# Optimization experiments

Hardware: AMD Instinct MI355X
Metric: run time of the kernel (lower is better)

The kernel has to match this reference:

```python
import jax, jax.numpy as jnp
import numpy as np

N = 8192
D = 512


def setup_inputs() -> dict:
    key = jax.random.key(0)
    ks = jax.random.split(key, 6)
    s = 1.0 / np.sqrt(D)
    return {
        "x": jax.random.normal(ks[0], (N, D), jnp.float32),
        "spatial_encoding": jax.random.normal(ks[1], (N, N), jnp.float32),
        "edge_encoding": jax.random.normal(ks[2], (N, N), jnp.float32),
        "Wq": jax.random.normal(ks[3], (D, D), jnp.float32) * s,
        "bq": jnp.zeros((D,), jnp.float32),
        "Wk": jax.random.normal(ks[4], (D, D), jnp.float32) * s,
        "bk": jnp.zeros((D,), jnp.float32),
        "Wv": jax.random.normal(ks[5], (D, D), jnp.float32) * s,
        "bv": jnp.zeros((D,), jnp.float32),
    }


def reference(x, spatial_encoding, edge_encoding, Wq, bq, Wk, bk, Wv, bv):
    # Linear layers (torch nn.Linear: y = x @ W.T + b)
    q = x @ Wq.T + bq  # [N, D]
    k = x @ Wk.T + bk  # [N, D]
    v = x @ Wv.T + bv  # [N, D]
    scale = 1.0 / jnp.sqrt(jnp.asarray(q.shape[-1], q.dtype))
    a = (q @ k.T) * scale + spatial_encoding + edge_encoding  # [N, N]
    attn = jax.nn.softmax(a, axis=-1)
    return attn @ v  # [N, D]
```

## Files before the change

### kernel.cpp

```cpp
#include <hip/hip_runtime.h>


constexpr int NT = 8192;
constexpr int DM = 512;
constexpr float SM_SHIFT = 12.0f;
constexpr float QSCALE = 0.04419417382415922f;

typedef _Float16 f16;
typedef _Float16 half8  __attribute__((ext_vector_type(8)));
typedef _Float16 half4v __attribute__((ext_vector_type(4)));
typedef float    float4v __attribute__((ext_vector_type(4)));

__device__ __forceinline__ void gload_lds16(const void* gsrc, void* ldst) {
  __builtin_amdgcn_global_load_lds(
      (const __attribute__((address_space(1))) void*)gsrc,
      (__attribute__((address_space(3))) void*)ldst, 16, 0, 0);
}

template<int ROWS>
__device__ __forceinline__ void stage32(const f16* __restrict__ g, int ldg,
                                        f16* l, int tid) {
  constexpr int ITERS = (ROWS * 4) / 256;
  #pragma unroll
  for (int c = 0; c < ITERS; ++c) {
    int lin = c * 256 + tid;
    gload_lds16(g + (size_t)(lin >> 2) * ldg + (lin & 3) * 8, l + lin * 8);
  }
}

__global__ __launch_bounds__(256) void k0_convert(
    const float* __restrict__ x, const float* __restrict__ wq,
    const float* __restrict__ wk, const float* __restrict__ wv,
    f16* __restrict__ xh, f16* __restrict__ wh) {
  int i = (blockIdx.x * 256 + threadIdx.x) * 4;
  const float* src; f16* dst; int off;
  if (i < NT * DM) { src = x; dst = xh; off = i; }
  else {
    int t = i - NT * DM;
    int w = t >> 18;
    off = t & ((1 << 18) - 1);
    src = (w == 0) ? wq : (w == 1) ? wk : wv;
    dst = wh + ((size_t)w << 18);
  }
  float4v v = *(const float4v*)(src + off);
  half4v h = { (f16)v.x, (f16)v.y, (f16)v.z, (f16)v.w };
  *(half4v*)(dst + off) = h;
}

__global__ __launch_bounds__(256) void k1_qkv(
    const f16* __restrict__ xh, const f16* __restrict__ wh,
    const float* __restrict__ bq, const float* __restrict__ bk,
    const float* __restrict__ bv,
    f16* __restrict__ qh, f16* __restrict__ kh, f16* __restrict__ vh) {
  __shared__ f16 As[128 * 32], Bs[128 * 32];
  int tid = threadIdx.x;
  int z = blockIdx.z;
  const f16* B0 = wh + (size_t)z * DM * DM;
  const float* bias = (z == 0) ? bq : (z == 1) ? bk : bv;
  f16* outp = (z == 0) ? qh : (z == 1) ? kh : vh;
  float scale = (z == 0) ? QSCALE : 1.0f;
  int i0 = blockIdx.y * 128, j0 = blockIdx.x * 128;
  int lane = tid & 63, warp = tid >> 6;
  int l15 = lane & 15, quad = lane >> 4;
  int wm = (warp >> 1) * 64, wn = (warp & 1) * 64;

  float4v acc[4][4] = {};
  const f16* Ag = xh + (size_t)i0 * DM;
  const f16* Bg = B0 + (size_t)j0 * DM;
  for (int kk = 0; kk < DM; kk += 32) {
    stage32<128>(Ag + kk, DM, As, tid);
    stage32<128>(Bg + kk, DM, Bs, tid);
    __syncthreads();
    half8 a[4], b[4];
    #pragma unroll
    for (int f = 0; f < 4; ++f)
      a[f] = *(const half8*)&As[(wm + f * 16 + l15) * 32 + quad * 8];
    #pragma unroll
    for (int f = 0; f < 4; ++f)
      b[f] = *(const half8*)&Bs[(wn + f * 16 + l15) * 32 + quad * 8];
    #pragma unroll
    for (int fm = 0; fm < 4; ++fm)
      #pragma unroll
      for (int fn = 0; fn < 4; ++fn)
        acc[fm][fn] = __builtin_amdgcn_mfma_f32_16x16x32_f16(
            a[fm], b[fn], acc[fm][fn], 0, 0, 0);
    __syncthreads();
  }
  #pragma unroll
  for (int fm = 0; fm < 4; ++fm)
    #pragma unroll
    for (int r = 0; r < 4; ++r) {
      int grow = i0 + wm + fm * 16 + quad * 4 + r;
      #pragma unroll
      for (int fn = 0; fn < 4; ++fn) {
        int gcol = j0 + wn + fn * 16 + l15;
        float v = (acc[fm][fn][r] + bias[gcol]) * scale;
        outp[(size_t)grow * DM + gcol] = (f16)v;
      }
    }
}

__global__ __launch_bounds__(256) void k15_transpose(
    const f16* __restrict__ v, f16* __restrict__ vT) {
  __shared__ f16 t[64][65];
  int bj = blockIdx.x * 64;
  int bi = blockIdx.y * 64;
  int tx = threadIdx.x & 63, ty = threadIdx.x >> 6;
  #pragma unroll
  for (int i = 0; i < 16; ++i)
    t[ty + i * 4][tx] = v[(size_t)(bi + ty + i * 4) * DM + bj + tx];
  __syncthreads();
  #pragma unroll
  for (int i = 0; i < 16; ++i)
    vT[(size_t)(bj + ty + i * 4) * NT + bi + tx] = t[tx][ty + i * 4];
}

constexpr int SLD = 132;

template<bool P16>
__global__ __launch_bounds__(256) void k2_scores(
    const f16* __restrict__ qh, const f16* __restrict__ kh,
    const float* __restrict__ spatial, const float* edge,
    f16* pOut16, float* pOut32, float* __restrict__ rowsum) {
  __shared__ __align__(16) char smem[32 * SLD * 4];
  f16* As = (f16*)smem;
  f16* Bs = (f16*)(smem + 8192);
  float* slab = (float*)smem;

  int tid = threadIdx.x;
  int i0 = blockIdx.y * 128, j0 = blockIdx.x * 128;
  int lane = tid & 63, warp = tid >> 6;
  int l15 = lane & 15, quad = lane >> 4;
  int wm = (warp >> 1) * 64, wn = (warp & 1) * 64;

  float4v acc[4][4] = {};
  const f16* Ag = qh + (size_t)i0 * DM;
  const f16* Bg = kh + (size_t)j0 * DM;
  for (int kk = 0; kk < DM; kk += 32) {
    stage32<128>(Ag + kk, DM, As, tid);
    stage32<128>(Bg + kk, DM, Bs, tid);
    __syncthreads();
    half8 a[4], b[4];
    #pragma unroll
    for (int f = 0; f < 4; ++f)
      a[f] = *(const half8*)&As[(wm + f * 16 + l15) * 32 + quad * 8];
    #pragma unroll
    for (int f = 0; f < 4; ++f)
      b[f] = *(const half8*)&Bs[(wn + f * 16 + l15) * 32 + quad * 8];
    #pragma unroll
    for (int fm = 0; fm < 4; ++fm)
      #pragma unroll
      for (int fn = 0; fn < 4; ++fn)
        acc[fm][fn] = __builtin_amdgcn_mfma_f32_16x16x32_f16(
            a[fm], b[fn], acc[fm][fn], 0, 0, 0);
    __syncthreads();
  }

  int rrow = tid >> 3;
  int col0 = (tid & 7) * 16;
  #pragma unroll
  for (int s = 0; s < 4; ++s) {
    if ((warp >> 1) == (s >> 1)) {
      int fmb = (s & 1) * 2;
      #pragma unroll
      for (int f = 0; f < 2; ++f)
        #pragma unroll
        for (int r = 0; r < 4; ++r) {
          int ris = f * 16 + quad * 4 + r;
          #pragma unroll
          for (int fn = 0; fn < 4; ++fn)
            slab[ris * SLD + wn + fn * 16 + l15] = acc[fmb + f][fn][r];
        }
    }
    __syncthreads();
    {
      int grow = i0 + s * 32 + rrow;
      size_t base = (size_t)grow * NT + j0 + col0;
      float4v sc[4], spv[4], egv[4];
      #pragma unroll
      for (int c = 0; c < 4; ++c) {
        sc[c]  = *(float4v*)&slab[rrow * SLD + col0 + c * 4];
        spv[c] = *(const float4v*)(spatial + base + c * 4);
        egv[c] = *(const float4v*)(edge + base + c * 4);
      }
      float rs = 0.f;
      if (P16) {
        half8 h[2];
        #pragma unroll
        for (int c = 0; c < 4; ++c)
          #pragma unroll
          for (int e = 0; e < 4; ++e) {
            float p = __expf(sc[c][e] + spv[c][e] + egv[c][e] - SM_SHIFT);
            rs += p;
            h[c >> 1][(c & 1) * 4 + e] = (f16)p;
          }
        *(half8*)(pOut16 + base) = h[0];
        *(half8*)(pOut16 + base + 8) = h[1];
      } else {
        #pragma unroll
        for (int c = 0; c < 4; ++c) {
          float4v pv;
          #pragma unroll
          for (int e = 0; e < 4; ++e) {
            float p = __expf(sc[c][e] + spv[c][e] + egv[c][e] - SM_SHIFT);
            rs += p;
            pv[e] = p;
          }
          *(float4v*)(pOut32 + base + c * 4) = pv;
        }
      }
      rs += __shfl_xor(rs, 1);
      rs += __shfl_xor(rs, 2);
      rs += __shfl_xor(rs, 4);
      if ((tid & 7) == 0) atomicAdd(&rowsum[grow], rs);
    }
    __syncthreads();
  }
}

template<bool P16>
__global__ __launch_bounds__(256) void k3_out(
    const f16* __restrict__ p16, const float* p32,
    const f16* __restrict__ vT, const float* __restrict__ rowsum,
    float* __restrict__ out) {
  __shared__ f16 As[2 * 64 * 32], Bs[2 * 128 * 32];
  int tid = threadIdx.x;
  int i0 = blockIdx.y * 64;
  int j0 = blockIdx.x * 128;
  int lane = tid & 63, warp = tid >> 6;
  int l15 = lane & 15, quad = lane >> 4;
  int wn = warp * 32;

  float4v acc[4][2] = {};
  const f16* Bg = vT + (size_t)j0 * NT;
  for (int kk = 0; kk < NT; kk += 64) {
    if (P16) {
      stage32<64>(p16 + (size_t)i0 * NT + kk, NT, As, tid);
      stage32<64>(p16 + (size_t)i0 * NT + kk + 32, NT, As + 64 * 32, tid);
    } else {
      #pragma unroll
      for (int sub = 0; sub < 2; ++sub) {
        int row = tid >> 2, cc = tid & 3;
        const float4v* src = (const float4v*)(
            p32 + (size_t)(i0 + row) * NT + kk + sub * 32 + cc * 8);
        float4v f0 = src[0], f1 = src[1];
        half8 h = { (f16)f0.x, (f16)f0.y, (f16)f0.z, (f16)f0.w,
                    (f16)f1.x, (f16)f1.y, (f16)f1.z, (f16)f1.w };
        *(half8*)&As[sub * 64 * 32 + tid * 8] = h;
      }
    }
    stage32<128>(Bg + kk, NT, Bs, tid);
    stage32<128>(Bg + kk + 32, NT, Bs + 128 * 32, tid);
    __syncthreads();
    #pragma unroll
    for (int sub = 0; sub < 2; ++sub) {
      half8 a[4], b[2];
      #pragma unroll
      for (int f = 0; f < 4; ++f)
        a[f] = *(const half8*)&As[sub * 2048 + (f * 16 + l15) * 32 + quad * 8];
      #pragma unroll
      for (int f = 0; f < 2; ++f)
        b[f] = *(const half8*)
            &Bs[sub * 4096 + (wn + f * 16 + l15) * 32 + quad * 8];
      #pragma unroll
      for (int fm = 0; fm < 4; ++fm)
        #pragma unroll
        for (int fn = 0; fn < 2; ++fn)
          acc[fm][fn] = __builtin_amdgcn_mfma_f32_16x16x32_f16(
              a[fm], b[fn], acc[fm][fn], 0, 0, 0);
    }
    __syncthreads();
  }
  #pragma unroll
  for (int fm = 0; fm < 4; ++fm)
    #pragma unroll
    for (int r = 0; r < 4; ++r) {
      int grow = i0 + fm * 16 + quad * 4 + r;
      float inv = 1.0f / rowsum[grow];
      #pragma unroll
      for (int fn = 0; fn < 2; ++fn) {
        int gcol = j0 + wn + fn * 16 + l15;
        out[(size_t)grow * DM + gcol] = acc[fm][fn][r] * inv;
      }
    }
}

extern "C" void kernel_launch(void* const* d_in, const int* in_sizes, int n_in,
                              void* d_out, int out_size, void* d_ws,
                              size_t ws_size, hipStream_t stream) {
  (void)in_sizes; (void)n_in; (void)out_size;
  const float* x  = (const float*)d_in[0];
  const float* sp = (const float*)d_in[1];
  float*       eg = (float*)d_in[2];
  const float* Wq = (const float*)d_in[3];
  const float* bq = (const float*)d_in[4];
  const float* Wk = (const float*)d_in[5];
  const float* bk = (const float*)d_in[6];
  const float* Wv = (const float*)d_in[7];
  const float* bv = (const float*)d_in[8];
  float* out = (float*)d_out;

  char* ws = (char*)d_ws;
  const size_t MB = 1ull << 20;
  f16* qh = (f16*)(ws + 0 * MB);
  f16* kh = (f16*)(ws + 8 * MB);
  f16* vh = (f16*)(ws + 16 * MB);
  f16* vT = (f16*)(ws + 24 * MB);
  f16* xh = (f16*)(ws + 32 * MB);
  f16* wh = (f16*)(ws + 40 * MB);
  float* rowsum = (float*)(ws + 42 * MB);
  f16* p16 = (f16*)(ws + 48 * MB);
  bool useP16 = ws_size >= 176 * MB;

  k0_convert<<<4864, 256, 0, stream>>>(x, Wq, Wk, Wv, xh, wh);
  (void)hipMemsetAsync(rowsum, 0, NT * sizeof(float), stream);
  k1_qkv<<<dim3(4, 64, 3), 256, 0, stream>>>(xh, wh, bq, bk, bv, qh, kh, vh);
  k15_transpose<<<dim3(8, 128), 256, 0, stream>>>(vh, vT);
  if (useP16) {
    k2_scores<true><<<dim3(64, 64), 256, 0, stream>>>(qh, kh, sp, eg, p16,
                                                      nullptr, rowsum);
    k3_out<true><<<dim3(4, 128), 256, 0, stream>>>(p16, nullptr, vT, rowsum,
                                                   out);
  } else {
    k2_scores<false><<<dim3(64, 64), 256, 0, stream>>>(qh, kh, sp, eg, nullptr,
                                                       eg, rowsum);
    k3_out<false><<<dim3(4, 128), 256, 0, stream>>>(nullptr, eg, vT, rowsum,
                                                    out);
  }
}
```

Measured before the change: 778.0 us.

## Overlap bias loads with QK MFMA loop and widen score/output kernels to 512 threads

The scores kernel now loads the spatial and edge bias tiles during the QK^T K-loop, pre-summing them into a 64KB LDS buffer. The exp/rowsum epilogue then reads accumulators directly, with no separate LDS slab pass. Both the scores and output GEMM kernels move to 512-thread blocks with smaller per-warp tiles, and the output kernel stages 128-wide K chunks via direct global-to-LDS loads. The aim is to hide the large bias read traffic behind matrix math. The cost is much higher LDS use per block and narrower, less coalesced probability stores.

```diff
diff --git a/kernel.cpp b/kernel.cpp
--- a/kernel.cpp
+++ b/kernel.cpp
@@ -52,7 +52,7 @@
     const float* __restrict__ bq, const float* __restrict__ bk,
     const float* __restrict__ bv,
     f16* __restrict__ qh, f16* __restrict__ kh, f16* __restrict__ vh) {
-  __shared__ f16 As[128 * 32], Bs[128 * 32];
+  __shared__ __align__(16) f16 As[128 * 32], Bs[128 * 32];
   int tid = threadIdx.x;
   int z = blockIdx.z;
   const f16* B0 = wh + (size_t)z * DM * DM;
@@ -115,159 +115,134 @@
     vT[(size_t)(bj + ty + i * 4) * NT + bi + tx] = t[tx][ty + i * 4];
 }
 
-constexpr int SLD = 132;
-
 template<bool P16>
-__global__ __launch_bounds__(256) void k2_scores(
+__global__ __launch_bounds__(512, 4) void k2_scores(
     const f16* __restrict__ qh, const f16* __restrict__ kh,
     const float* __restrict__ spatial, const float* edge,
     f16* pOut16, float* pOut32, float* __restrict__ rowsum) {
-  __shared__ __align__(16) char smem[32 * SLD * 4];
-  f16* As = (f16*)smem;
-  f16* Bs = (f16*)(smem + 8192);
-  float* slab = (float*)smem;
+  __shared__ __align__(16) f16 As[128 * 32], Bs[128 * 32];
+  __shared__ __align__(16) float E[128 * 128];
 
   int tid = threadIdx.x;
   int i0 = blockIdx.y * 128, j0 = blockIdx.x * 128;
   int lane = tid & 63, warp = tid >> 6;
   int l15 = lane & 15, quad = lane >> 4;
-  int wm = (warp >> 1) * 64, wn = (warp & 1) * 64;
-
-  float4v acc[4][4] = {};
+  int wm = (warp >> 2) * 64, wn = (warp & 3) * 32;
+
+  float4v acc[4][2] = {};
   const f16* Ag = qh + (size_t)i0 * DM;
   const f16* Bg = kh + (size_t)j0 * DM;
-  for (int kk = 0; kk < DM; kk += 32) {
-    stage32<128>(Ag + kk, DM, As, tid);
-    stage32<128>(Bg + kk, DM, Bs, tid);
-    __syncthreads();
-    half8 a[4], b[4];
+  int arow = tid >> 2, achk = (tid & 3) * 8;
+  for (int c = 0; c < 16; ++c) {
+    int kk = c * 32;
+    gload_lds16(Ag + (size_t)arow * DM + kk + achk, As + tid * 8);
+    gload_lds16(Bg + (size_t)arow * DM + kk + achk, Bs + tid * 8);
+    float4v spv, egv;
+    int erow = 0, ecol = 0;
+    bool eload = (c & 1) == 0;
+    if (eload) {
+      erow = c * 8 + (tid >> 5);
+      ecol = (tid & 31) * 4;
+      size_t gb = (size_t)(i0 + erow) * NT + j0 + ecol;
+      spv = *(const float4v*)(spatial + gb);
+      egv = *(const float4v*)(edge + gb);
+    }
+    __syncthreads();
+    half8 a[4], b[2];
     #pragma unroll
     for (int f = 0; f < 4; ++f)
       a[f] = *(const half8*)&As[(wm + f * 16 + l15) * 32 + quad * 8];
     #pragma unroll
-    for (int f = 0; f < 4; ++f)
+    for (int f = 0; f < 2; ++f)
       b[f] = *(const half8*)&Bs[(wn + f * 16 + l15) * 32 + quad * 8];
     #pragma unroll
     for (int fm = 0; fm < 4; ++fm)
       #pragma unroll
-      for (int fn = 0; fn < 4; ++fn)
+      for (int fn = 0; fn < 2; ++fn)
         acc[fm][fn] = __builtin_amdgcn_mfma_f32_16x16x32_f16(
             a[fm], b[fn], acc[fm][fn], 0, 0, 0);
-    __syncthreads();
-  }
-
-  int rrow = tid >> 3;
-  int col0 = (tid & 7) * 16;
-  #pragma unroll
-  for (int s = 0; s < 4; ++s) {
-    if ((warp >> 1) == (s >> 1)) {
-      int fmb = (s & 1) * 2;
-      #pragma unroll
-      for (int f = 0; f < 2; ++f)
-        #pragma unroll
-        for (int r = 0; r < 4; ++r) {
-          int ris = f * 16 + quad * 4 + r;
-          #pragma unroll
-          for (int fn = 0; fn < 4; ++fn)
-            slab[ris * SLD + wn + fn * 16 + l15] = acc[fmb + f][fn][r];
-        }
-    }
-    __syncthreads();
-    {
-      int grow = i0 + s * 32 + rrow;
-      size_t base = (size_t)grow * NT + j0 + col0;
-      float4v sc[4], spv[4], egv[4];
-      #pragma unroll
-      for (int c = 0; c < 4; ++c) {
-        sc[c]  = *(float4v*)&slab[rrow * SLD + col0 + c * 4];
-        spv[c] = *(const float4v*)(spatial + base + c * 4);
-        egv[c] = *(const float4v*)(edge + base + c * 4);
-      }
+    if (eload)
+      *(float4v*)&E[erow * 128 + ecol] = spv + egv;
+    __syncthreads();
+  }
+
+  #pragma unroll
+  for (int fm = 0; fm < 4; ++fm)
+    #pragma unroll
+    for (int r = 0; r < 4; ++r) {
+      int lrow = wm + fm * 16 + quad * 4 + r;
+      int grow = i0 + lrow;
+      size_t gbase = (size_t)grow * NT + j0;
       float rs = 0.f;
-      if (P16) {
-        half8 h[2];
-        #pragma unroll
-        for (int c = 0; c < 4; ++c)
-          #pragma unroll
-          for (int e = 0; e < 4; ++e) {
-            float p = __expf(sc[c][e] + spv[c][e] + egv[c][e] - SM_SHIFT);
-            rs += p;
-            h[c >> 1][(c & 1) * 4 + e] = (f16)p;
-          }
-        *(half8*)(pOut16 + base) = h[0];
-        *(half8*)(pOut16 + base + 8) = h[1];
-      } else {
-        #pragma unroll
-        for (int c = 0; c < 4; ++c) {
-          float4v pv;
-          #pragma unroll
-          for (int e = 0; e < 4; ++e) {
-            float p = __expf(sc[c][e] + spv[c][e] + egv[c][e] - SM_SHIFT);
-            rs += p;
-            pv[e] = p;
-          }
-          *(float4v*)(pOut32 + base + c * 4) = pv;
-        }
+      #pragma unroll
+      for (int fn = 0; fn < 2; ++fn) {
+        int lcol = wn + fn * 16 + l15;
+        float p = __expf(acc[fm][fn][r] + E[lrow * 128 + lcol] - SM_SHIFT);
+        rs += p;
+        if (P16) pOut16[gbase + lcol] = (f16)p;
+        else     pOut32[gbase + lcol] = p;
       }
       rs += __shfl_xor(rs, 1);
       rs += __shfl_xor(rs, 2);
       rs += __shfl_xor(rs, 4);
-      if ((tid & 7) == 0) atomicAdd(&rowsum[grow], rs);
-    }
-    __syncthreads();
-  }
+      rs += __shfl_xor(rs, 8);
+      if (l15 == 0) atomicAdd(&rowsum[grow], rs);
+    }
 }
 
 template<bool P16>
-__global__ __launch_bounds__(256) void k3_out(
+__global__ __launch_bounds__(512, 4) void k3_out(
     const f16* __restrict__ p16, const float* p32,
     const f16* __restrict__ vT, const float* __restrict__ rowsum,
     float* __restrict__ out) {
-  __shared__ f16 As[2 * 64 * 32], Bs[2 * 128 * 32];
+  __shared__ __align__(16) f16 As[4 * 64 * 32];
+  __shared__ __align__(16) f16 Bs[4 * 128 * 32];
   int tid = threadIdx.x;
   int i0 = blockIdx.y * 64;
   int j0 = blockIdx.x * 128;
   int lane = tid & 63, warp = tid >> 6;
   int l15 = lane & 15, quad = lane >> 4;
-  int wn = warp * 32;
-
-  float4v acc[4][2] = {};
-  const f16* Bg = vT + (size_t)j0 * NT;
-  for (int kk = 0; kk < NT; kk += 64) {
+  int wn = warp * 16;
+
+  float4v acc[4] = {};
+  for (int kk = 0; kk < NT; kk += 128) {
     if (P16) {
-      stage32<64>(p16 + (size_t)i0 * NT + kk, NT, As, tid);
-      stage32<64>(p16 + (size_t)i0 * NT + kk + 32, NT, As + 64 * 32, tid);
+      #pragma unroll
+      for (int pass = 0; pass < 2; ++pass) {
+        int slot = pass * 512 + tid, s = slot >> 8, lin = slot & 255;
+        gload_lds16(p16 + (size_t)(i0 + (lin >> 2)) * NT + kk + s * 32
+                        + (lin & 3) * 8,
+                    As + s * 2048 + lin * 8);
+      }
     } else {
       #pragma unroll
-      for (int sub = 0; sub < 2; ++sub) {
-        int row = tid >> 2, cc = tid & 3;
+      for (int pass = 0; pass < 2; ++pass) {
+        int slot = pass * 512 + tid, s = slot >> 8, lin = slot & 255;
         const float4v* src = (const float4v*)(
-            p32 + (size_t)(i0 + row) * NT + kk + sub * 32 + cc * 8);
+            p32 + (size_t)(i0 + (lin >> 2)) * NT + kk + s * 32 + (lin & 3) * 8);
         float4v f0 = src[0], f1 = src[1];
         half8 h = { (f16)f0.x, (f16)f0.y, (f16)f0.z, (f16)f0.w,
                     (f16)f1.x, (f16)f1.y, (f16)f1.z, (f16)f1.w };
-        *(half8*)&As[sub * 64 * 32 + tid * 8] = h;
+        *(half8*)&As[s * 2048 + lin * 8] = h;
       }
     }
-    stage32<128>(Bg + kk, NT, Bs, tid);
-    stage32<128>(Bg + kk + 32, NT, Bs + 128 * 32, tid);
-    __syncthreads();
-    #pragma unroll
-    for (int sub = 0; sub < 2; ++sub) {
-      half8 a[4], b[2];
+    #pragma unroll
+    for (int s = 0; s < 4; ++s)
+      gload_lds16(vT + (size_t)(j0 + (tid >> 2)) * NT + kk + s * 32
+                      + (tid & 3) * 8,
+                  Bs + s * 4096 + tid * 8);
+    __syncthreads();
+    #pragma unroll
+    for (int s = 0; s < 4; ++s) {
+      half8 a[4], b;
       #pragma unroll
       for (int f = 0; f < 4; ++f)
-        a[f] = *(const half8*)&As[sub * 2048 + (f * 16 + l15) * 32 + quad * 8];
-      #pragma unroll
-      for (int f = 0; f < 2; ++f)
-        b[f] = *(const half8*)
-            &Bs[sub * 4096 + (wn + f * 16 + l15) * 32 + quad * 8];
+        a[f] = *(const half8*)&As[s * 2048 + (f * 16 + l15) * 32 + quad * 8];
+      b = *(const half8*)&Bs[s * 4096 + (wn + l15) * 32 + quad * 8];
       #pragma unroll
       for (int fm = 0; fm < 4; ++fm)
-        #pragma unroll
-        for (int fn = 0; fn < 2; ++fn)
-          acc[fm][fn] = __builtin_amdgcn_mfma_f32_16x16x32_f16(
-              a[fm], b[fn], acc[fm][fn], 0, 0, 0);
+        acc[fm] = __builtin_amdgcn_mfma_f32_16x16x32_f16(a[fm], b, acc[fm],
+                                                         0, 0, 0);
     }
     __syncthreads();
   }
@@ -277,11 +252,7 @@
     for (int r = 0; r < 4; ++r) {
       int grow = i0 + fm * 16 + quad * 4 + r;
       float inv = 1.0f / rowsum[grow];
-      #pragma unroll
-      for (int fn = 0; fn < 2; ++fn) {
-        int gcol = j0 + wn + fn * 16 + l15;
-        out[(size_t)grow * DM + gcol] = acc[fm][fn][r] * inv;
-      }
+      out[(size_t)grow * DM + j0 + wn + l15] = acc[fm][r] * inv;
     }
 }
 
@@ -317,14 +288,14 @@
   k1_qkv<<<dim3(4, 64, 3), 256, 0, stream>>>(xh, wh, bq, bk, bv, qh, kh, vh);
   k15_transpose<<<dim3(8, 128), 256, 0, stream>>>(vh, vT);
   if (useP16) {
-    k2_scores<true><<<dim3(64, 64), 256, 0, stream>>>(qh, kh, sp, eg, p16,
+    k2_scores<true><<<dim3(64, 64), 512, 0, stream>>>(qh, kh, sp, eg, p16,
                                                       nullptr, rowsum);
-    k3_out<true><<<dim3(4, 128), 256, 0, stream>>>(p16, nullptr, vT, rowsum,
+    k3_out<true><<<dim3(4, 128), 512, 0, stream>>>(p16, nullptr, vT, rowsum,
                                                    out);
   } else {
-    k2_scores<false><<<dim3(64, 64), 256, 0, stream>>>(qh, kh, sp, eg, nullptr,
+    k2_scores<false><<<dim3(64, 64), 512, 0, stream>>>(qh, kh, sp, eg, nullptr,
                                                        eg, rowsum);
-    k3_out<false><<<dim3(4, 128), 256, 0, stream>>>(nullptr, eg, vT, rowsum,
+    k3_out<false><<<dim3(4, 128), 512, 0, stream>>>(nullptr, eg, vT, rowsum,
                                                     out);
   }
 }
```

Result: slower. 855.2 us (+9.9%).
